# Kernel optimization log

Measured on AMD Instinct MI355X. Metric: run time of the kernel, lower is better.

## Reference

```python
import jax, jax.numpy as jnp
import numpy as np

N_NODES = 100000
N_EDGES = 1600000
DIMS = [(2, 128), (128, 128), (128, 32), (32, 32), (32, 32)]


def setup_inputs() -> dict:
    key = jax.random.key(0)
    ks = jax.random.split(key, 2 + 3 * len(DIMS) + 2)
    x = jax.random.normal(ks[0], (N_NODES, 2), dtype=jnp.float32)
    edge_index = jax.random.randint(ks[1], (2, N_EDGES), 0, N_NODES, dtype=jnp.int32)
    inp = {"x": x, "edge_index": edge_index, "batch_size": 100}
    k = 2
    for i, (cin, cout) in enumerate(DIMS, start=1):
        s = 1.0 / np.sqrt(cin)
        inp[f"Wl{i}"] = jax.random.normal(ks[k], (cin, cout), dtype=jnp.float32) * s; k += 1
        inp[f"bl{i}"] = jnp.zeros((cout,), dtype=jnp.float32)
        inp[f"Wr{i}"] = jax.random.normal(ks[k], (cin, cout), dtype=jnp.float32) * s; k += 1
    inp["W_out"] = jax.random.normal(ks[k], (32, 1), dtype=jnp.float32) * (1.0 / np.sqrt(32.0)); k += 1
    inp["b_out"] = jnp.zeros((1,), dtype=jnp.float32)
    return inp


def reference(x, edge_index, batch_size,
              Wl1, bl1, Wr1, Wl2, bl2, Wr2, Wl3, bl3, Wr3,
              Wl4, bl4, Wr4, Wl5, bl5, Wr5, W_out, b_out):
    src, dst = edge_index[0], edge_index[1]
    h = x.reshape(-1, 2)
    n = h.shape[0]
    # in-degree per target node, clamped to 1 (PyG mean aggr gives 0 for isolated nodes)
    deg = jax.ops.segment_sum(jnp.ones_like(src, dtype=h.dtype), dst, num_segments=n)
    inv_deg = (1.0 / jnp.maximum(deg, 1.0))[:, None]

    def sage(h, Wl, bl, Wr):
        # mean-aggregate neighbor features, then SAGEConv: lin_l(agg) + lin_r(h)
        agg = jax.ops.segment_sum(h[src], dst, num_segments=n) * inv_deg
        return agg @ Wl + bl + h @ Wr

    for Wl, bl, Wr in ((Wl1, bl1, Wr1), (Wl2, bl2, Wr2), (Wl3, bl3, Wr3),
                       (Wl4, bl4, Wr4), (Wl5, bl5, Wr5)):
        h = jax.nn.relu(sage(h, Wl, bl, Wr))
    # dropout is identity in eval mode
    out = h @ W_out + b_out  # [n, 1]
    return out.reshape(batch_size, -1)
```

## Files before the change

### kernel.cpp

```cpp
#include <hip/hip_runtime.h>
#include <hip/hip_bf16.h>

#define N_NODES 100000
#define N_EDGES 1600000
#define NBUCK 256
#define NODES_PER_BUCKET 391
#define EDGES_PER_CHUNK (N_EDGES / NBUCK)
#define FILL_LDS_CAP 8192

typedef __bf16 bf16x8 __attribute__((ext_vector_type(8)));
typedef float f32x4 __attribute__((ext_vector_type(4)));


__device__ inline unsigned short f2bf_rne(float v) {
    unsigned u = __float_as_uint(v);
    u += 0x7fffu + ((u >> 16) & 1u);
    return (unsigned short)(u >> 16);
}

__device__ inline unsigned pack_bf(float a, float b) {
    return (unsigned)f2bf_rne(a) | ((unsigned)f2bf_rne(b) << 16);
}

__device__ inline void acc8_bf(float* a, uint4 p) {
    a[0] += __uint_as_float(p.x << 16);
    a[1] += __uint_as_float(p.x & 0xffff0000u);
    a[2] += __uint_as_float(p.y << 16);
    a[3] += __uint_as_float(p.y & 0xffff0000u);
    a[4] += __uint_as_float(p.z << 16);
    a[5] += __uint_as_float(p.z & 0xffff0000u);
    a[6] += __uint_as_float(p.w << 16);
    a[7] += __uint_as_float(p.w & 0xffff0000u);
}


__global__ __launch_bounds__(256) void pa_count(const int* __restrict__ dst,
                                                int* __restrict__ blkCntT) {
    __shared__ int hist[NBUCK];
    hist[threadIdx.x] = 0;
    __syncthreads();
    int b0 = blockIdx.x * EDGES_PER_CHUNK;
    int b1 = min(b0 + EDGES_PER_CHUNK, N_EDGES);
    for (int i = b0 + (int)threadIdx.x; i < b1; i += 256) {
        int d = __builtin_nontemporal_load(&dst[i]);
        atomicAdd(&hist[d / NODES_PER_BUCKET], 1);
    }
    __syncthreads();
    blkCntT[threadIdx.x * NBUCK + blockIdx.x] = hist[threadIdx.x];
}

__global__ __launch_bounds__(256) void pa_scan1(const int* __restrict__ blkCntT,
                                                int* __restrict__ blkBaseL,
                                                int* __restrict__ bucketTotal) {
    __shared__ int s[256];
    int t = threadIdx.x;
    int v = blkCntT[blockIdx.x * NBUCK + t];
    s[t] = v;
    __syncthreads();
    for (int off = 1; off < 256; off <<= 1) {
        int u = (t >= off) ? s[t - off] : 0;
        __syncthreads();
        s[t] += u;
        __syncthreads();
    }
    blkBaseL[blockIdx.x * NBUCK + t] = s[t] - v;
    if (t == 255) bucketTotal[blockIdx.x] = s[255];
}

__global__ __launch_bounds__(256) void pa_scan2(const int* __restrict__ bucketTotal,
                                                int* __restrict__ bstart,
                                                int* __restrict__ offsets) {
    __shared__ int s[256];
    int t = threadIdx.x;
    int v = bucketTotal[t];
    s[t] = v;
    __syncthreads();
    for (int off = 1; off < 256; off <<= 1) {
        int u = (t >= off) ? s[t - off] : 0;
        __syncthreads();
        s[t] += u;
        __syncthreads();
    }
    bstart[t] = s[t] - v;
    if (t == 255) {
        bstart[256] = s[255];
        offsets[N_NODES] = s[255];
    }
}

__global__ __launch_bounds__(256) void pa_scatter(const int* __restrict__ src,
                                                  const int* __restrict__ dst,
                                                  const int* __restrict__ blkCntT,
                                                  const int* __restrict__ blkBaseL,
                                                  const int* __restrict__ bstart,
                                                  int2* __restrict__ staging) {
    __shared__ int runStart[NBUCK];
    __shared__ int cur[NBUCK];
    __shared__ int gbase[NBUCK];
    __shared__ int2 buf[EDGES_PER_CHUNK];

    const int tid = threadIdx.x;
    const int g = blockIdx.x;
    const int b0 = g * EDGES_PER_CHUNK;
    const int b1 = min(b0 + EDGES_PER_CHUNK, N_EDGES);

    {
        __shared__ int s[256];
        int v = blkCntT[tid * NBUCK + g];
        s[tid] = v;
        __syncthreads();
        for (int off = 1; off < 256; off <<= 1) {
            int u = (tid >= off) ? s[tid - off] : 0;
            __syncthreads();
            s[tid] += u;
            __syncthreads();
        }
        runStart[tid] = s[tid] - v;
        cur[tid] = s[tid] - v;
        gbase[tid] = bstart[tid] + blkBaseL[tid * NBUCK + g];
    }
    __syncthreads();
    for (int i = b0 + tid; i < b1; i += 256) {
        int d = __builtin_nontemporal_load(&dst[i]);
        int s_ = __builtin_nontemporal_load(&src[i]);
        int k = d / NODES_PER_BUCKET;
        int p = atomicAdd(&cur[k], 1);
        buf[p] = make_int2(s_, d);
    }
    __syncthreads();
    int cnt = b1 - b0;
    for (int i = tid; i < cnt; i += 256) {
        int2 e = buf[i];
        int k = e.y / NODES_PER_BUCKET;
        staging[gbase[k] + (i - runStart[k])] = e;
    }
}

__global__ __launch_bounds__(512) void pc_fill(const int2* __restrict__ staging,
                                               const int* __restrict__ bstart,
                                               int* __restrict__ ssrc,
                                               int* __restrict__ offsets,
                                               float* __restrict__ inv_deg) {
    __shared__ int scnt[NODES_PER_BUCKET];
    __shared__ int sexc[NODES_PER_BUCKET];
    __shared__ int scur[NODES_PER_BUCKET];
    __shared__ int ssrcL[FILL_LDS_CAP];

    const int tid = threadIdx.x;
    const int b = blockIdx.x;
    const int node0 = b * NODES_PER_BUCKET;
    const int nn = min(node0 + NODES_PER_BUCKET, N_NODES) - node0;
    if (nn <= 0) return;
    const int es = bstart[b], ee = bstart[b + 1];
    const int cnt = ee - es;

    for (int j = tid; j < nn; j += 512) scnt[j] = 0;
    __syncthreads();
    for (int i = es + tid; i < ee; i += 512) {
        int2 e = staging[i];
        atomicAdd(&scnt[e.y - node0], 1);
    }
    __syncthreads();

    if (tid < 64) {
        int base = tid * 7;
        int vals[7];
        int run = 0;
#pragma unroll
        for (int j = 0; j < 7; ++j) {
            int idx = base + j;
            int c = (idx < nn) ? scnt[idx] : 0;
            vals[j] = run;
            run += c;
        }
        int inc = run;
#pragma unroll
        for (int off = 1; off < 64; off <<= 1) {
            int u = __shfl_up(inc, off, 64);
            if (tid >= off) inc += u;
        }
        int laneExcl = inc - run;
#pragma unroll
        for (int j = 0; j < 7; ++j) {
            int idx = base + j;
            if (idx < nn) sexc[idx] = laneExcl + vals[j];
        }
    }
    __syncthreads();

    for (int j = tid; j < nn; j += 512) {
        int c = scnt[j];
        int ex = sexc[j];
        offsets[node0 + j] = es + ex;
        inv_deg[node0 + j] = 1.0f / (float)max(c, 1);
        scur[j] = ex;
    }
    __syncthreads();

    if (cnt <= FILL_LDS_CAP) {
        for (int i = es + tid; i < ee; i += 512) {
            int2 e = staging[i];
            int p = atomicAdd(&scur[e.y - node0], 1);
            ssrcL[p] = e.x;
        }
        __syncthreads();
        for (int i = tid; i < cnt; i += 512) ssrc[es + i] = ssrcL[i];
    } else {
        for (int i = es + tid; i < ee; i += 512) {
            int2 e = staging[i];
            int p = atomicAdd(&scur[e.y - node0], 1);
            ssrc[es + p] = e.x;
        }
    }
}


__global__ __launch_bounds__(256) void aggregate_bf128(const unsigned short* __restrict__ hb,
                                                       const int* __restrict__ offs,
                                                       const int* __restrict__ ssrc,
                                                       const float* __restrict__ inv_deg,
                                                       unsigned short* __restrict__ aggb,
                                                       int nnodes) {
    int t = blockIdx.x * 256 + threadIdx.x;
    if (t >= nnodes * 16) return;
    int node = t >> 4;
    int c = t & 15;
    int b = offs[node], e = offs[node + 1];
    const uint4* __restrict__ hb4 = (const uint4*)hb;
    float acc[8] = {0.f, 0.f, 0.f, 0.f, 0.f, 0.f, 0.f, 0.f};
    int i = b;
    for (; i + 4 <= e; i += 4) {
        uint4 p0 = hb4[(size_t)ssrc[i] * 16 + c];
        uint4 p1 = hb4[(size_t)ssrc[i + 1] * 16 + c];
        uint4 p2 = hb4[(size_t)ssrc[i + 2] * 16 + c];
        uint4 p3 = hb4[(size_t)ssrc[i + 3] * 16 + c];
        acc8_bf(acc, p0);
        acc8_bf(acc, p1);
        acc8_bf(acc, p2);
        acc8_bf(acc, p3);
    }
    for (; i < e; ++i) {
        uint4 p = hb4[(size_t)ssrc[i] * 16 + c];
        acc8_bf(acc, p);
    }
    float s = inv_deg[node];
    uint4 o;
    o.x = pack_bf(acc[0] * s, acc[1] * s);
    o.y = pack_bf(acc[2] * s, acc[3] * s);
    o.z = pack_bf(acc[4] * s, acc[5] * s);
    o.w = pack_bf(acc[6] * s, acc[7] * s);
    ((uint4*)aggb)[t] = o;
}

__global__ __launch_bounds__(256) void aggregate2(const float* __restrict__ h,
                                                  const int* __restrict__ offs,
                                                  const int* __restrict__ ssrc,
                                                  const float* __restrict__ inv_deg,
                                                  float* __restrict__ agg, int nnodes) {
    int node = blockIdx.x * blockDim.x + threadIdx.x;
    if (node >= nnodes) return;
    int b = offs[node], e = offs[node + 1];
    const float2* __restrict__ h2 = (const float2*)h;
    float2 a0 = make_float2(0.f, 0.f), a1 = make_float2(0.f, 0.f);
    int i = b;
    for (; i + 2 <= e; i += 2) {
        float2 v = h2[ssrc[i]];
        float2 w = h2[ssrc[i + 1]];
        a0.x += v.x; a0.y += v.y;
        a1.x += w.x; a1.y += w.y;
    }
    if (i < e) {
        float2 v = h2[ssrc[i]];
        a0.x += v.x; a0.y += v.y;
    }
    float s = inv_deg[node];
    ((float2*)agg)[node] = make_float2((a0.x + a1.x) * s, (a0.y + a1.y) * s);
}


__global__ __launch_bounds__(256) void prep_all(const float* __restrict__ Wl2,
                                                const float* __restrict__ Wr2,
                                                const float* __restrict__ Wl3,
                                                const float* __restrict__ Wr3,
                                                const float* __restrict__ Wl4,
                                                const float* __restrict__ Wr4,
                                                const float* __restrict__ Wl5,
                                                const float* __restrict__ Wr5,
                                                unsigned short* __restrict__ Wt,
                                                unsigned short* __restrict__ W3c,
                                                unsigned short* __restrict__ W4c,
                                                unsigned short* __restrict__ W5c) {
    int idx = blockIdx.x * 256 + threadIdx.x;
    if (idx < 32768) {
        int n = idx >> 8, k = idx & 255;
        float v = (k < 128) ? Wl2[k * 128 + n] : Wr2[(k - 128) * 128 + n];
        Wt[idx] = f2bf_rne(v);
    } else if (idx < 32768 + 8192) {
        int j = idx - 32768;
        int n = j >> 7, k = j & 127;
        float v = (n < 32) ? Wl3[k * 32 + n] : Wr3[k * 32 + (n - 32)];
        W3c[j] = f2bf_rne(v);
    } else if (idx < 32768 + 8192 + 2048) {
        int j = idx - 32768 - 8192;
        int n = j >> 5, k = j & 31;
        float v = (n < 32) ? Wl4[k * 32 + n] : Wr4[k * 32 + (n - 32)];
        W4c[j] = f2bf_rne(v);
    } else if (idx < 32768 + 8192 + 4096) {
        int j = idx - 32768 - 8192 - 2048;
        int n = j >> 5, k = j & 31;
        float v = (n < 32) ? Wl5[k * 32 + n] : Wr5[k * 32 + (n - 32)];
        W5c[j] = f2bf_rne(v);
    }
}


__global__ __launch_bounds__(256) void gemm_l2_mfma(const unsigned short* __restrict__ Ab,
                                                    const unsigned short* __restrict__ Hb,
                                                    const unsigned short* __restrict__ Wt,
                                                    const float* __restrict__ bias,
                                                    const unsigned short* __restrict__ W3c,
                                                    unsigned short* __restrict__ g3b,
                                                    float* __restrict__ p3, int M) {
    constexpr int BM = 128, BK = 64;
    __shared__ unsigned short smem[26112];
#define SA(r, c) smem[(r) * 72 + (c)]
#define SB(r, c) smem[9216 + (r) * 72 + (c)]
#define SH(r, c) smem[(r) * 136 + (c)]
#define SW3(r, c) smem[17408 + (r) * 136 + (c)]

    const int tid = threadIdx.x;
    const int m0 = blockIdx.x * BM;
    const int lane = tid & 63;
    const int wid = tid >> 6;
    const int l15 = lane & 15;
    const int quad = lane >> 4;
    const int wm = (wid >> 1) * 64;
    const int wn = (wid & 1) * 64;

    f32x4 acc[4][4];
#pragma unroll
    for (int i = 0; i < 4; ++i)
#pragma unroll
        for (int j = 0; j < 4; ++j) acc[i][j] = (f32x4){0.f, 0.f, 0.f, 0.f};

    for (int k0 = 0; k0 < 256; k0 += BK) {
        const uint4* __restrict__ srcA = (const uint4*)((k0 < 128) ? Ab : Hb);
        const int kc = (k0 & 64) >> 3;
#pragma unroll
        for (int l = 0; l < 4; ++l) {
            int idx = tid + l * 256;
            int row = idx >> 3;
            int c8 = idx & 7;
            int gr = min(m0 + row, M - 1);
            uint4 va = srcA[(size_t)gr * 16 + kc + c8];
            *(uint4*)&SA(row, c8 * 8) = va;
            uint4 vb = ((const uint4*)Wt)[(size_t)row * 32 + (k0 >> 3) + c8];
            *(uint4*)&SB(row, c8 * 8) = vb;
        }
        __syncthreads();

#pragma unroll
        for (int ks = 0; ks < BK; ks += 32) {
            bf16x8 a[4], b[4];
#pragma unroll
            for (int t = 0; t < 4; ++t) {
                a[t] = *(const bf16x8*)&SA(wm + t * 16 + l15, ks + quad * 8);
                b[t] = *(const bf16x8*)&SB(wn + t * 16 + l15, ks + quad * 8);
            }
#pragma unroll
            for (int i = 0; i < 4; ++i)
#pragma unroll
                for (int j = 0; j < 4; ++j)
                    acc[i][j] = __builtin_amdgcn_mfma_f32_16x16x32_bf16(
                        a[i], b[j], acc[i][j], 0, 0, 0);
        }
        __syncthreads();
    }

#pragma unroll
    for (int j = 0; j < 4; ++j) {
        int n = wn + j * 16 + l15;
        float bv = bias[n];
#pragma unroll
        for (int i = 0; i < 4; ++i) {
#pragma unroll
            for (int r = 0; r < 4; ++r) {
                int ml = wm + i * 16 + quad * 4 + r;
                SH(ml, n) = f2bf_rne(fmaxf(acc[i][j][r] + bv, 0.f));
            }
        }
    }
#pragma unroll
    for (int l = 0; l < 4; ++l) {
        int idx = tid + l * 256;
        int row = idx >> 4;
        int c8 = idx & 15;
        uint4 v = ((const uint4*)W3c)[(size_t)row * 16 + c8];
        *(uint4*)&SW3(row, c8 * 8) = v;
    }
    __syncthreads();

    f32x4 acc2[2][4];
#pragma unroll
    for (int i = 0; i < 2; ++i)
#pragma unroll
        for (int j = 0; j < 4; ++j) acc2[i][j] = (f32x4){0.f, 0.f, 0.f, 0.f};

#pragma unroll
    for (int ks = 0; ks < 128; ks += 32) {
        bf16x8 a[2], b[4];
#pragma unroll
        for (int i = 0; i < 2; ++i)
            a[i] = *(const bf16x8*)&SH(wid * 32 + i * 16 + l15, ks + quad * 8);
#pragma unroll
        for (int j = 0; j < 4; ++j)
            b[j] = *(const bf16x8*)&SW3(j * 16 + l15, ks + quad * 8);
#pragma unroll
        for (int i = 0; i < 2; ++i)
#pragma unroll
            for (int j = 0; j < 4; ++j)
                acc2[i][j] = __builtin_amdgcn_mfma_f32_16x16x32_bf16(
                    a[i], b[j], acc2[i][j], 0, 0, 0);
    }

#pragma unroll
    for (int i = 0; i < 2; ++i) {
#pragma unroll
        for (int r = 0; r < 4; ++r) {
            int m = m0 + wid * 32 + i * 16 + quad * 4 + r;
            if (m >= M) continue;
#pragma unroll
            for (int j = 0; j < 4; ++j) {
                float v = acc2[i][j][r];
                if (j < 2) g3b[(size_t)m * 32 + j * 16 + l15] = f2bf_rne(v);
                else       p3[(size_t)m * 32 + (j - 2) * 16 + l15] = v;
            }
        }
    }
#undef SA
#undef SB
#undef SH
#undef SW3
}


__global__ __launch_bounds__(256) void aggregate_combine32(
        const unsigned short* __restrict__ gb_prev,
        const int* __restrict__ offs,
        const int* __restrict__ ssrc,
        const float* __restrict__ inv_deg,
        const float* __restrict__ p,
        const float* __restrict__ bias,
        const unsigned short* __restrict__ Wc,
        unsigned short* __restrict__ g_next,
        float* __restrict__ p_next, int nnodes) {
    __shared__ unsigned short hB[64][40];
    __shared__ unsigned short wB[64][40];

    const int tid = threadIdx.x;
    const int node0 = blockIdx.x * 64;
    const int node = node0 + (tid >> 2);
    const int c = tid & 3;
    const int ln = tid >> 2;

#pragma unroll
    for (int l = 0; l < 2; ++l) {
        int id = tid + l * 256;
        int r = id >> 3, cc = id & 7;
        uint2 v = ((const uint2*)Wc)[(size_t)r * 8 + cc];
        *(uint2*)&wB[r][cc * 4] = v;
    }

    uint4 hout = make_uint4(0u, 0u, 0u, 0u);
    if (node < nnodes) {
        int b = offs[node], e = offs[node + 1];
        const uint4* __restrict__ hb4 = (const uint4*)gb_prev;
        float acc[8] = {0.f, 0.f, 0.f, 0.f, 0.f, 0.f, 0.f, 0.f};
        int i = b;
        for (; i + 4 <= e; i += 4) {
            uint4 p0 = hb4[(size_t)ssrc[i] * 4 + c];
            uint4 p1 = hb4[(size_t)ssrc[i + 1] * 4 + c];
            uint4 p2 = hb4[(size_t)ssrc[i + 2] * 4 + c];
            uint4 p3 = hb4[(size_t)ssrc[i + 3] * 4 + c];
            acc8_bf(acc, p0);
            acc8_bf(acc, p1);
            acc8_bf(acc, p2);
            acc8_bf(acc, p3);
        }
        for (; i < e; ++i) acc8_bf(acc, hb4[(size_t)ssrc[i] * 4 + c]);
        float s = inv_deg[node];
        const float4* prow = (const float4*)(p + (size_t)node * 32 + c * 8);
        float4 p0 = prow[0], p1 = prow[1];
        const float* bb = bias + c * 8;
        float h0 = fmaxf(acc[0] * s + p0.x + bb[0], 0.f);
        float h1 = fmaxf(acc[1] * s + p0.y + bb[1], 0.f);
        float h2 = fmaxf(acc[2] * s + p0.z + bb[2], 0.f);
        float h3 = fmaxf(acc[3] * s + p0.w + bb[3], 0.f);
        float h4 = fmaxf(acc[4] * s + p1.x + bb[4], 0.f);
        float h5 = fmaxf(acc[5] * s + p1.y + bb[5], 0.f);
        float h6 = fmaxf(acc[6] * s + p1.z + bb[6], 0.f);
        float h7 = fmaxf(acc[7] * s + p1.w + bb[7], 0.f);
        hout.x = pack_bf(h0, h1);
        hout.y = pack_bf(h2, h3);
        hout.z = pack_bf(h4, h5);
        hout.w = pack_bf(h6, h7);
    }
    *(uint4*)&hB[ln][c * 8] = hout;
    __syncthreads();

    const int lane = tid & 63;
    const int wid = tid >> 6;
    const int l15 = lane & 15;
    const int quad = lane >> 4;

    bf16x8 a = *(const bf16x8*)&hB[wid * 16 + l15][quad * 8];
    f32x4 accm[4];
#pragma unroll
    for (int j = 0; j < 4; ++j) {
        bf16x8 b = *(const bf16x8*)&wB[j * 16 + l15][quad * 8];
        accm[j] = __builtin_amdgcn_mfma_f32_16x16x32_bf16(
            a, b, (f32x4){0.f, 0.f, 0.f, 0.f}, 0, 0, 0);
    }

#pragma unroll
    for (int r = 0; r < 4; ++r) {
        int m = node0 + wid * 16 + quad * 4 + r;
        if (m >= nnodes) continue;
#pragma unroll
        for (int j = 0; j < 4; ++j) {
            float v = accm[j][r];
            if (j < 2) g_next[(size_t)m * 32 + j * 16 + l15] = f2bf_rne(v);
            else       p_next[(size_t)m * 32 + (j - 2) * 16 + l15] = v;
        }
    }
}

__global__ __launch_bounds__(256) void aggregate_final32(
        const unsigned short* __restrict__ gb_prev,
        const int* __restrict__ offs,
        const int* __restrict__ ssrc,
        const float* __restrict__ inv_deg,
        const float* __restrict__ p,
        const float* __restrict__ bias,
        const float* __restrict__ Wout,
        const float* __restrict__ bout,
        float* __restrict__ out, int nnodes) {
    int t = blockIdx.x * 256 + threadIdx.x;
    int node = t >> 2;
    int c = t & 3;
    if (node >= nnodes) return;
    int b = offs[node], e = offs[node + 1];
    const uint4* __restrict__ hb4 = (const uint4*)gb_prev;
    float acc[8] = {0.f, 0.f, 0.f, 0.f, 0.f, 0.f, 0.f, 0.f};
    int i = b;
    for (; i + 4 <= e; i += 4) {
        uint4 p0 = hb4[(size_t)ssrc[i] * 4 + c];
        uint4 p1 = hb4[(size_t)ssrc[i + 1] * 4 + c];
        uint4 p2 = hb4[(size_t)ssrc[i + 2] * 4 + c];
        uint4 p3 = hb4[(size_t)ssrc[i + 3] * 4 + c];
        acc8_bf(acc, p0);
        acc8_bf(acc, p1);
        acc8_bf(acc, p2);
        acc8_bf(acc, p3);
    }
    for (; i < e; ++i) acc8_bf(acc, hb4[(size_t)ssrc[i] * 4 + c]);
    float s = inv_deg[node];
    const float4* prow = (const float4*)(p + (size_t)node * 32 + c * 8);
    float4 p0 = prow[0], p1 = prow[1];
    const float* bb = bias + c * 8;
    const float* w = Wout + c * 8;
    float sum = 0.f;
    sum = fmaf(fmaxf(acc[0] * s + p0.x + bb[0], 0.f), w[0], sum);
    sum = fmaf(fmaxf(acc[1] * s + p0.y + bb[1], 0.f), w[1], sum);
    sum = fmaf(fmaxf(acc[2] * s + p0.z + bb[2], 0.f), w[2], sum);
    sum = fmaf(fmaxf(acc[3] * s + p0.w + bb[3], 0.f), w[3], sum);
    sum = fmaf(fmaxf(acc[4] * s + p1.x + bb[4], 0.f), w[4], sum);
    sum = fmaf(fmaxf(acc[5] * s + p1.y + bb[5], 0.f), w[5], sum);
    sum = fmaf(fmaxf(acc[6] * s + p1.z + bb[6], 0.f), w[6], sum);
    sum = fmaf(fmaxf(acc[7] * s + p1.w + bb[7], 0.f), w[7], sum);
    sum += __shfl_down(sum, 2, 4);
    sum += __shfl_down(sum, 1, 4);
    if (c == 0) out[node] = sum + bout[0];
}

__global__ __launch_bounds__(256) void sage_linear2(const float* __restrict__ agg,
                                                    const float* __restrict__ h,
                                                    const float* __restrict__ Wl,
                                                    const float* __restrict__ bl,
                                                    const float* __restrict__ Wr,
                                                    unsigned short* __restrict__ out_bf,
                                                    int nnodes) {
    constexpr int Cout = 128;
    int t = blockIdx.x * blockDim.x + threadIdx.x;
    if (t >= nnodes * Cout) return;
    int node = t / Cout;
    int c = t - node * Cout;
    float2 a = ((const float2*)agg)[node];
    float2 hh = ((const float2*)h)[node];
    float acc = bl[c];
    acc = fmaf(a.x, Wl[c], acc);
    acc = fmaf(a.y, Wl[Cout + c], acc);
    acc = fmaf(hh.x, Wr[c], acc);
    acc = fmaf(hh.y, Wr[Cout + c], acc);
    acc = fmaxf(acc, 0.f);
    out_bf[t] = f2bf_rne(acc);
}


extern "C" void kernel_launch(void* const* d_in, const int* in_sizes, int n_in,
                              void* d_out, int out_size, void* d_ws, size_t ws_size,
                              hipStream_t stream) {
    const float* x      = (const float*)d_in[0];
    const int*   ei     = (const int*)d_in[1];
    const float* Wl1    = (const float*)d_in[3];
    const float* bl1    = (const float*)d_in[4];
    const float* Wr1    = (const float*)d_in[5];
    const float* Wl2    = (const float*)d_in[6];
    const float* bl2    = (const float*)d_in[7];
    const float* Wr2    = (const float*)d_in[8];
    const float* Wl3    = (const float*)d_in[9];
    const float* bl3    = (const float*)d_in[10];
    const float* Wr3    = (const float*)d_in[11];
    const float* Wl4    = (const float*)d_in[12];
    const float* bl4    = (const float*)d_in[13];
    const float* Wr4    = (const float*)d_in[14];
    const float* Wl5    = (const float*)d_in[15];
    const float* bl5    = (const float*)d_in[16];
    const float* Wr5    = (const float*)d_in[17];
    const float* W_out  = (const float*)d_in[18];
    const float* b_out  = (const float*)d_in[19];
    float* out = (float*)d_out;

    const int N = N_NODES, E = N_EDGES;
    const int* e_src = ei;
    const int* e_dst = ei + E;

    size_t off = 0;
    auto carve = [&](size_t bytes) {
        void* p = (char*)d_ws + off;
        off += (bytes + 255) & ~(size_t)255;
        return p;
    };
    int*   offsets  = (int*)carve((size_t)(N + 1) * 4);
    float* inv_deg  = (float*)carve((size_t)N * 4);
    int*   ssrc     = (int*)carve((size_t)E * 4);
    int*   blkCntT  = (int*)carve((size_t)NBUCK * NBUCK * 4);
    int*   blkBaseL = (int*)carve((size_t)NBUCK * NBUCK * 4);
    int*   bucketTotal = (int*)carve((size_t)NBUCK * 4);
    int*   bstart   = (int*)carve((size_t)(NBUCK + 1) * 4);
    int2*  staging  = (int2*)carve((size_t)E * 8);
    unsigned short* Wt  = (unsigned short*)carve((size_t)128 * 256 * 2);
    unsigned short* W3c = (unsigned short*)carve((size_t)64 * 128 * 2);
    unsigned short* W4c = (unsigned short*)carve((size_t)64 * 32 * 2);
    unsigned short* W5c = (unsigned short*)carve((size_t)64 * 32 * 2);
    float* agg      = (float*)carve((size_t)N * 128 * 4);
    float* bufA     = (float*)carve((size_t)N * 128 * 4);
    unsigned short* g3b = (unsigned short*)carve((size_t)N * 32 * 2);
    unsigned short* g4b = (unsigned short*)carve((size_t)N * 32 * 2);
    unsigned short* g5b = (unsigned short*)carve((size_t)N * 32 * 2);

    float* slotA = agg;
    float* slotC = agg + (size_t)N * 64;
    unsigned short* h1_bf = (unsigned short*)bufA;
    unsigned short* aggB  = (unsigned short*)bufA + (size_t)N * 128;

    pa_count<<<NBUCK, 256, 0, stream>>>(e_dst, blkCntT);
    pa_scan1<<<NBUCK, 256, 0, stream>>>(blkCntT, blkBaseL, bucketTotal);
    pa_scan2<<<1, 256, 0, stream>>>(bucketTotal, bstart, offsets);
    pa_scatter<<<NBUCK, 256, 0, stream>>>(e_src, e_dst, blkCntT, blkBaseL, bstart, staging);
    pc_fill<<<NBUCK, 512, 0, stream>>>(staging, bstart, ssrc, offsets, inv_deg);
    prep_all<<<176, 256, 0, stream>>>(Wl2, Wr2, Wl3, Wr3, Wl4, Wr4, Wl5, Wr5,
                                      Wt, W3c, W4c, W5c);

    const int gemm_grid = (N + 127) / 128;
    const int comb_grid = (N + 63) / 64;

    aggregate2<<<(N + 255) / 256, 256, 0, stream>>>(x, offsets, ssrc, inv_deg, slotC, N);
    sage_linear2<<<(N * 128 + 255) / 256, 256, 0, stream>>>(slotC, x, Wl1, bl1, Wr1, h1_bf, N);

    aggregate_bf128<<<(N * 16 + 255) / 256, 256, 0, stream>>>(h1_bf, offsets, ssrc,
                                                              inv_deg, aggB, N);
    gemm_l2_mfma<<<gemm_grid, 256, 0, stream>>>(aggB, h1_bf, Wt, bl2, W3c, g3b, slotA, N);

    aggregate_combine32<<<comb_grid, 256, 0, stream>>>(g3b, offsets, ssrc, inv_deg,
                                                       slotA, bl3, W4c, g4b, slotC, N);

    aggregate_combine32<<<comb_grid, 256, 0, stream>>>(g4b, offsets, ssrc, inv_deg,
                                                       slotC, bl4, W5c, g5b, slotA, N);

    aggregate_final32<<<(N * 4 + 255) / 256, 256, 0, stream>>>(g5b, offsets, ssrc, inv_deg,
                                                               slotA, bl5, W_out, b_out,
                                                               out, N);
}
```

Measured before the change: 341.9 us.

## Fuse CSR build into one cooperative kernel and fuse layer-1 aggregate+linear

Replaces the count/scan/scan/scatter/fill CSR construction kernels with a single cooperative kernel that uses grid.sync between phases and keeps the edge chunk in LDS instead of re-reading src/dst. Also merges the layer-1 neighbor aggregation and 2->128 linear transform into one kernel with 4 threads per node, avoiding the intermediate aggregate buffer. This removes several launches and global round-trips, at the cost of grid-wide barriers and a large LDS footprint per block.

```diff
diff --git a/kernel.cpp b/kernel.cpp
--- a/kernel.cpp
+++ b/kernel.cpp
@@ -1,5 +1,8 @@
 #include <hip/hip_runtime.h>
 #include <hip/hip_bf16.h>
+#include <hip/hip_cooperative_groups.h>
+
+namespace cg = cooperative_groups;
 
 #define N_NODES 100000
 #define N_EDGES 1600000
@@ -34,125 +37,119 @@
 }
 
 
-__global__ __launch_bounds__(256) void pa_count(const int* __restrict__ dst,
-                                                int* __restrict__ blkCntT) {
-    __shared__ int hist[NBUCK];
-    hist[threadIdx.x] = 0;
-    __syncthreads();
-    int b0 = blockIdx.x * EDGES_PER_CHUNK;
-    int b1 = min(b0 + EDGES_PER_CHUNK, N_EDGES);
-    for (int i = b0 + (int)threadIdx.x; i < b1; i += 256) {
-        int d = __builtin_nontemporal_load(&dst[i]);
-        atomicAdd(&hist[d / NODES_PER_BUCKET], 1);
-    }
-    __syncthreads();
-    blkCntT[threadIdx.x * NBUCK + blockIdx.x] = hist[threadIdx.x];
-}
-
-__global__ __launch_bounds__(256) void pa_scan1(const int* __restrict__ blkCntT,
+__global__ __launch_bounds__(512) void csr_coop(const int* __restrict__ src,
+                                                const int* __restrict__ dst,
+                                                int* __restrict__ blkCntT,
                                                 int* __restrict__ blkBaseL,
-                                                int* __restrict__ bucketTotal) {
-    __shared__ int s[256];
-    int t = threadIdx.x;
-    int v = blkCntT[blockIdx.x * NBUCK + t];
-    s[t] = v;
-    __syncthreads();
-    for (int off = 1; off < 256; off <<= 1) {
-        int u = (t >= off) ? s[t - off] : 0;
-        __syncthreads();
-        s[t] += u;
-        __syncthreads();
-    }
-    blkBaseL[blockIdx.x * NBUCK + t] = s[t] - v;
-    if (t == 255) bucketTotal[blockIdx.x] = s[255];
-}
-
-__global__ __launch_bounds__(256) void pa_scan2(const int* __restrict__ bucketTotal,
+                                                int* __restrict__ bucketTotal,
                                                 int* __restrict__ bstart,
-                                                int* __restrict__ offsets) {
-    __shared__ int s[256];
-    int t = threadIdx.x;
-    int v = bucketTotal[t];
-    s[t] = v;
-    __syncthreads();
-    for (int off = 1; off < 256; off <<= 1) {
-        int u = (t >= off) ? s[t - off] : 0;
-        __syncthreads();
-        s[t] += u;
-        __syncthreads();
-    }
-    bstart[t] = s[t] - v;
-    if (t == 255) {
-        bstart[256] = s[255];
-        offsets[N_NODES] = s[255];
-    }
-}
-
-__global__ __launch_bounds__(256) void pa_scatter(const int* __restrict__ src,
-                                                  const int* __restrict__ dst,
-                                                  const int* __restrict__ blkCntT,
-                                                  const int* __restrict__ blkBaseL,
-                                                  const int* __restrict__ bstart,
-                                                  int2* __restrict__ staging) {
-    __shared__ int runStart[NBUCK];
-    __shared__ int cur[NBUCK];
-    __shared__ int gbase[NBUCK];
-    __shared__ int2 buf[EDGES_PER_CHUNK];
-
+                                                int2* __restrict__ staging,
+                                                int* __restrict__ ssrc,
+                                                int* __restrict__ offsets,
+                                                float* __restrict__ inv_deg) {
+    __shared__ __align__(16) char smem[106496];
+    int2* bufRaw   = (int2*)smem;
+    int2* bufSrt   = (int2*)(smem + 50000);
+    int*  hist     = (int*)(smem + 100000);
+    int*  runStart = (int*)(smem + 101024);
+    int*  cur      = (int*)(smem + 102048);
+    int*  gbase    = (int*)(smem + 103072);
+    int*  sscan    = (int*)(smem + 104096);
+
+    cg::grid_group grid = cg::this_grid();
     const int tid = threadIdx.x;
     const int g = blockIdx.x;
     const int b0 = g * EDGES_PER_CHUNK;
     const int b1 = min(b0 + EDGES_PER_CHUNK, N_EDGES);
-
-    {
-        __shared__ int s[256];
-        int v = blkCntT[tid * NBUCK + g];
-        s[tid] = v;
-        __syncthreads();
-        for (int off = 1; off < 256; off <<= 1) {
-            int u = (tid >= off) ? s[tid - off] : 0;
+    const int cnt = b1 - b0;
+
+    if (tid < NBUCK) hist[tid] = 0;
+    __syncthreads();
+    for (int i = b0 + tid; i < b1; i += 512) {
+        int d = dst[i];
+        int s = src[i];
+        bufRaw[i - b0] = make_int2(s, d);
+        atomicAdd(&hist[d / NODES_PER_BUCKET], 1);
+    }
+    __syncthreads();
+    if (tid < NBUCK) blkCntT[(size_t)g * NBUCK + tid] = hist[tid];
+    __threadfence();
+    grid.sync();
+
+    if (tid < NBUCK) sscan[tid] = blkCntT[(size_t)tid * NBUCK + g];
+    __syncthreads();
+    for (int off = 1; off < NBUCK; off <<= 1) {
+        int u = (tid >= off && tid < NBUCK) ? sscan[tid - off] : 0;
+        __syncthreads();
+        if (tid < NBUCK) sscan[tid] += u;
+        __syncthreads();
+    }
+    if (tid < NBUCK) {
+        int v = blkCntT[(size_t)tid * NBUCK + g];
+        blkBaseL[(size_t)g * NBUCK + tid] = sscan[tid] - v;
+    }
+    if (tid == NBUCK - 1) bucketTotal[g] = sscan[NBUCK - 1];
+    __threadfence();
+    grid.sync();
+
+    if (g == 0) {
+        if (tid < NBUCK) sscan[tid] = bucketTotal[tid];
+        __syncthreads();
+        for (int off = 1; off < NBUCK; off <<= 1) {
+            int u = (tid >= off && tid < NBUCK) ? sscan[tid - off] : 0;
             __syncthreads();
-            s[tid] += u;
+            if (tid < NBUCK) sscan[tid] += u;
             __syncthreads();
         }
-        runStart[tid] = s[tid] - v;
-        cur[tid] = s[tid] - v;
-        gbase[tid] = bstart[tid] + blkBaseL[tid * NBUCK + g];
-    }
-    __syncthreads();
-    for (int i = b0 + tid; i < b1; i += 256) {
-        int d = __builtin_nontemporal_load(&dst[i]);
-        int s_ = __builtin_nontemporal_load(&src[i]);
-        int k = d / NODES_PER_BUCKET;
+        if (tid < NBUCK) bstart[tid] = sscan[tid] - bucketTotal[tid];
+        if (tid == NBUCK - 1) {
+            bstart[NBUCK] = sscan[NBUCK - 1];
+            offsets[N_NODES] = sscan[NBUCK - 1];
+        }
+        __threadfence();
+    }
+    grid.sync();
+
+    if (tid < NBUCK) sscan[tid] = hist[tid];
+    __syncthreads();
+    for (int off = 1; off < NBUCK; off <<= 1) {
+        int u = (tid >= off && tid < NBUCK) ? sscan[tid - off] : 0;
+        __syncthreads();
+        if (tid < NBUCK) sscan[tid] += u;
+        __syncthreads();
+    }
+    if (tid < NBUCK) {
+        int v = hist[tid];
+        runStart[tid] = sscan[tid] - v;
+        cur[tid] = sscan[tid] - v;
+        gbase[tid] = bstart[tid] + blkBaseL[(size_t)tid * NBUCK + g];
+    }
+    __syncthreads();
+    for (int i = tid; i < cnt; i += 512) {
+        int2 e = bufRaw[i];
+        int k = e.y / NODES_PER_BUCKET;
         int p = atomicAdd(&cur[k], 1);
-        buf[p] = make_int2(s_, d);
-    }
-    __syncthreads();
-    int cnt = b1 - b0;
-    for (int i = tid; i < cnt; i += 256) {
-        int2 e = buf[i];
+        bufSrt[p] = e;
+    }
+    __syncthreads();
+    for (int i = tid; i < cnt; i += 512) {
+        int2 e = bufSrt[i];
         int k = e.y / NODES_PER_BUCKET;
         staging[gbase[k] + (i - runStart[k])] = e;
     }
-}
-
-__global__ __launch_bounds__(512) void pc_fill(const int2* __restrict__ staging,
-                                               const int* __restrict__ bstart,
-                                               int* __restrict__ ssrc,
-                                               int* __restrict__ offsets,
-                                               float* __restrict__ inv_deg) {
-    __shared__ int scnt[NODES_PER_BUCKET];
-    __shared__ int sexc[NODES_PER_BUCKET];
-    __shared__ int scur[NODES_PER_BUCKET];
-    __shared__ int ssrcL[FILL_LDS_CAP];
-
-    const int tid = threadIdx.x;
-    const int b = blockIdx.x;
-    const int node0 = b * NODES_PER_BUCKET;
+    __threadfence();
+    grid.sync();
+
+    int* scnt  = (int*)smem;
+    int* sexc  = (int*)(smem + 1600);
+    int* scur  = (int*)(smem + 3200);
+    int* ssrcL = (int*)(smem + 4800);
+
+    const int node0 = g * NODES_PER_BUCKET;
     const int nn = min(node0 + NODES_PER_BUCKET, N_NODES) - node0;
     if (nn <= 0) return;
-    const int es = bstart[b], ee = bstart[b + 1];
-    const int cnt = ee - es;
+    const int es = bstart[g], ee = bstart[g + 1];
+    const int ecnt = ee - es;
 
     for (int j = tid; j < nn; j += 512) scnt[j] = 0;
     __syncthreads();
@@ -197,20 +194,71 @@
     }
     __syncthreads();
 
-    if (cnt <= FILL_LDS_CAP) {
+    if (ecnt <= FILL_LDS_CAP) {
         for (int i = es + tid; i < ee; i += 512) {
             int2 e = staging[i];
             int p = atomicAdd(&scur[e.y - node0], 1);
             ssrcL[p] = e.x;
         }
         __syncthreads();
-        for (int i = tid; i < cnt; i += 512) ssrc[es + i] = ssrcL[i];
+        for (int i = tid; i < ecnt; i += 512) ssrc[es + i] = ssrcL[i];
     } else {
         for (int i = es + tid; i < ee; i += 512) {
             int2 e = staging[i];
             int p = atomicAdd(&scur[e.y - node0], 1);
             ssrc[es + p] = e.x;
         }
+    }
+}
+
+
+__global__ __launch_bounds__(256) void sage1_fused(const float* __restrict__ x,
+                                                   const int* __restrict__ offs,
+                                                   const int* __restrict__ ssrc,
+                                                   const float* __restrict__ inv_deg,
+                                                   const float* __restrict__ Wl,
+                                                   const float* __restrict__ bl,
+                                                   const float* __restrict__ Wr,
+                                                   unsigned short* __restrict__ out_bf,
+                                                   int nnodes) {
+    int t = blockIdx.x * 256 + threadIdx.x;
+    int node = t >> 2;
+    int c = t & 3;
+    if (node >= nnodes) return;
+    const float2* __restrict__ x2 = (const float2*)x;
+    int b = offs[node], e = offs[node + 1];
+    float ax = 0.f, ay = 0.f;
+    for (int i = b + c; i < e; i += 4) {
+        float2 v = x2[ssrc[i]];
+        ax += v.x;
+        ay += v.y;
+    }
+    ax += __shfl_xor(ax, 1, 4);
+    ay += __shfl_xor(ay, 1, 4);
+    ax += __shfl_xor(ax, 2, 4);
+    ay += __shfl_xor(ay, 2, 4);
+    float s = inv_deg[node];
+    ax *= s; ay *= s;
+    float2 hh = x2[node];
+    const float* wl0 = Wl + c * 32;
+    const float* wl1 = Wl + 128 + c * 32;
+    const float* wr0 = Wr + c * 32;
+    const float* wr1 = Wr + 128 + c * 32;
+    const float* bb = bl + c * 32;
+    uint4* dst4 = (uint4*)(out_bf + (size_t)node * 128 + c * 32);
+#pragma unroll
+    for (int q = 0; q < 4; ++q) {
+        unsigned vals[4];
+#pragma unroll
+        for (int pj = 0; pj < 4; ++pj) {
+            int j = q * 8 + pj * 2;
+            float v0 = fmaxf(bb[j] + ax * wl0[j] + ay * wl1[j] +
+                             hh.x * wr0[j] + hh.y * wr1[j], 0.f);
+            float v1 = fmaxf(bb[j + 1] + ax * wl0[j + 1] + ay * wl1[j + 1] +
+                             hh.x * wr0[j + 1] + hh.y * wr1[j + 1], 0.f);
+            vals[pj] = pack_bf(v0, v1);
+        }
+        dst4[q] = make_uint4(vals[0], vals[1], vals[2], vals[3]);
     }
 }
 
@@ -250,31 +298,6 @@
     o.z = pack_bf(acc[4] * s, acc[5] * s);
     o.w = pack_bf(acc[6] * s, acc[7] * s);
     ((uint4*)aggb)[t] = o;
-}
-
-__global__ __launch_bounds__(256) void aggregate2(const float* __restrict__ h,
-                                                  const int* __restrict__ offs,
-                                                  const int* __restrict__ ssrc,
-                                                  const float* __restrict__ inv_deg,
-                                                  float* __restrict__ agg, int nnodes) {
-    int node = blockIdx.x * blockDim.x + threadIdx.x;
-    if (node >= nnodes) return;
-    int b = offs[node], e = offs[node + 1];
-    const float2* __restrict__ h2 = (const float2*)h;
-    float2 a0 = make_float2(0.f, 0.f), a1 = make_float2(0.f, 0.f);
-    int i = b;
-    for (; i + 2 <= e; i += 2) {
-        float2 v = h2[ssrc[i]];
-        float2 w = h2[ssrc[i + 1]];
-        a0.x += v.x; a0.y += v.y;
-        a1.x += w.x; a1.y += w.y;
-    }
-    if (i < e) {
-        float2 v = h2[ssrc[i]];
-        a0.x += v.x; a0.y += v.y;
-    }
-    float s = inv_deg[node];
-    ((float2*)agg)[node] = make_float2((a0.x + a1.x) * s, (a0.y + a1.y) * s);
 }
 
 
@@ -583,29 +606,6 @@
     if (c == 0) out[node] = sum + bout[0];
 }
 
-__global__ __launch_bounds__(256) void sage_linear2(const float* __restrict__ agg,
-                                                    const float* __restrict__ h,
-                                                    const float* __restrict__ Wl,
-                                                    const float* __restrict__ bl,
-                                                    const float* __restrict__ Wr,
-                                                    unsigned short* __restrict__ out_bf,
-                                                    int nnodes) {
-    constexpr int Cout = 128;
-    int t = blockIdx.x * blockDim.x + threadIdx.x;
-    if (t >= nnodes * Cout) return;
-    int node = t / Cout;
-    int c = t - node * Cout;
-    float2 a = ((const float2*)agg)[node];
-    float2 hh = ((const float2*)h)[node];
-    float acc = bl[c];
-    acc = fmaf(a.x, Wl[c], acc);
-    acc = fmaf(a.y, Wl[Cout + c], acc);
-    acc = fmaf(hh.x, Wr[c], acc);
-    acc = fmaf(hh.y, Wr[Cout + c], acc);
-    acc = fmaxf(acc, 0.f);
-    out_bf[t] = f2bf_rne(acc);
-}
-
 
 extern "C" void kernel_launch(void* const* d_in, const int* in_sizes, int n_in,
                               void* d_out, int out_size, void* d_ws, size_t ws_size,
@@ -664,19 +664,22 @@
     unsigned short* h1_bf = (unsigned short*)bufA;
     unsigned short* aggB  = (unsigned short*)bufA + (size_t)N * 128;
 
-    pa_count<<<NBUCK, 256, 0, stream>>>(e_dst, blkCntT);
-    pa_scan1<<<NBUCK, 256, 0, stream>>>(blkCntT, blkBaseL, bucketTotal);
-    pa_scan2<<<1, 256, 0, stream>>>(bucketTotal, bstart, offsets);
-    pa_scatter<<<NBUCK, 256, 0, stream>>>(e_src, e_dst, blkCntT, blkBaseL, bstart, staging);
-    pc_fill<<<NBUCK, 512, 0, stream>>>(staging, bstart, ssrc, offsets, inv_deg);
+    {
+        void* kargs[] = {(void*)&e_src, (void*)&e_dst, (void*)&blkCntT,
+                         (void*)&blkBaseL, (void*)&bucketTotal, (void*)&bstart,
+                         (void*)&staging, (void*)&ssrc, (void*)&offsets,
+                         (void*)&inv_deg};
+        hipLaunchCooperativeKernel((void*)csr_coop, dim3(NBUCK), dim3(512),
+                                   kargs, 0, stream);
+    }
     prep_all<<<176, 256, 0, stream>>>(Wl2, Wr2, Wl3, Wr3, Wl4, Wr4, Wl5, Wr5,
                                       Wt, W3c, W4c, W5c);
 
     const int gemm_grid = (N + 127) / 128;
     const int comb_grid = (N + 63) / 64;
 
-    aggregate2<<<(N + 255) / 256, 256, 0, stream>>>(x, offsets, ssrc, inv_deg, slotC, N);
-    sage_linear2<<<(N * 128 + 255) / 256, 256, 0, stream>>>(slotC, x, Wl1, bl1, Wr1, h1_bf, N);
+    sage1_fused<<<(N * 4 + 255) / 256, 256, 0, stream>>>(x, offsets, ssrc, inv_deg,
+                                                         Wl1, bl1, Wr1, h1_bf, N);
 
     aggregate_bf128<<<(N * 16 + 255) / 256, 256, 0, stream>>>(h1_bf, offsets, ssrc,
                                                               inv_deg, aggB, N);
```

Result: slower. 592.3 us (+73.2%).
